# Optimization experiments

Measured on AMD Instinct MI355X. Metric: run time of the kernel, lower is better.

Reference implementation:

```python
import jax, jax.numpy as jnp
import numpy as np

DIM = 64

def conv2d_g2(x, w, b):
    # 3x3 conv, padding=1, groups=2, NCHW
    y = jax.lax.conv_general_dilated(x, w, (1, 1), [(1, 1), (1, 1)],
                                     dimension_numbers=('NCHW', 'OIHW', 'NCHW'),
                                     feature_group_count=2)
    return y + b[None, :, None, None]

def bilinear_gather(x, py, px):
    # x: [B,C,H,W]; py,px: [B,K,H,W] float sample coords -> [B,K,H,W,C]
    B, C, H, W = x.shape
    y0 = jnp.floor(py); x0 = jnp.floor(px)
    ly = py - y0; lx = px - x0
    hy = 1.0 - ly; hx = 1.0 - lx
    b_idx = jnp.arange(B)[:, None, None, None]
    def gather(yi, xi):
        valid = (yi >= 0) & (yi < H) & (xi >= 0) & (xi < W)
        yc = jnp.clip(yi, 0, H - 1).astype(jnp.int32)
        xc = jnp.clip(xi, 0, W - 1).astype(jnp.int32)
        v = x[b_idx, :, yc, xc]  # [B,K,H,W,C]
        return v * valid[..., None].astype(x.dtype)
    return (gather(y0, x0) * (hy * hx)[..., None]
            + gather(y0, x0 + 1) * (hy * lx)[..., None]
            + gather(y0 + 1, x0) * (ly * hx)[..., None]
            + gather(y0 + 1, x0 + 1) * (ly * lx)[..., None])

def deform_dw(x, offset, w, b, k, pad, dil):
    # depthwise (groups=C, offset_groups=1) deformable conv, stride 1
    B, C, H, W = x.shape
    K = k * k
    off = offset.reshape(B, K, 2, H, W)  # torchvision layout: (dy,dx) per kernel tap
    ky = jnp.repeat(jnp.arange(k), k).astype(x.dtype)   # [K]
    kx = jnp.tile(jnp.arange(k), k).astype(x.dtype)     # [K]
    base_y = jnp.arange(H, dtype=x.dtype)[None, None, :, None] - pad + dil * ky[None, :, None, None]
    base_x = jnp.arange(W, dtype=x.dtype)[None, None, None, :] - pad + dil * kx[None, :, None, None]
    py = base_y + off[:, :, 0]  # [B,K,H,W]
    px = base_x + off[:, :, 1]
    val = bilinear_gather(x, py, px)  # [B,K,H,W,C]
    return jnp.einsum('bkhwc,ck->bchw', val, w.reshape(C, K)) + b[None, :, None, None]

def lsk_forward(x, w_off3, b_off3, w_off2, b_off2, w7, b7, w5, b5):
    B, C, H, W = x.shape
    offset3 = conv2d_g2(x, w_off3, b_off3)            # [B,98,H,W]
    out1 = deform_dw(x, offset3, w7, b7, 7, 9, 3)     # [B,C,H,W]
    offset2 = conv2d_g2(x, w_off2, b_off2)            # [B,50,H,W]
    out2 = deform_dw(out1, offset2, w5, b5, 5, 6, 3)  # [B,C,H,W]
    feats = jnp.stack([out1, out2], axis=1)           # [B,2,C,H,W]
    gap = feats.mean(axis=(3, 4), keepdims=True)      # [B,2,C,1,1]
    attn = jax.nn.softmax(gap, axis=1)
    return jnp.sum(feats * attn, axis=1)              # [B,C,H,W]

def setup_inputs() -> dict:
    key = jax.random.key(0)
    ks = jax.random.split(key, 9)
    B, C, H, W = 4, DIM, 56, 56
    return {
        'x':      jax.random.normal(ks[0], (B, C, H, W), jnp.float32),
        'w_off3': jax.random.normal(ks[1], (98, C // 2, 3, 3), jnp.float32) * 0.05,
        'b_off3': jax.random.normal(ks[2], (98,), jnp.float32) * 0.05,
        'w_off2': jax.random.normal(ks[3], (50, C // 2, 3, 3), jnp.float32) * 0.05,
        'b_off2': jax.random.normal(ks[4], (50,), jnp.float32) * 0.05,
        'w7':     jax.random.normal(ks[5], (C, 1, 7, 7), jnp.float32) * 0.1,
        'b7':     jax.random.normal(ks[6], (C,), jnp.float32) * 0.05,
        'w5':     jax.random.normal(ks[7], (C, 1, 5, 5), jnp.float32) * 0.1,
        'b5':     jax.random.normal(ks[8], (C,), jnp.float32) * 0.05,
    }

def reference(x, w_off3, b_off3, w_off2, b_off2, w7, b7, w5, b5):
    return lsk_forward(x, w_off3, b_off3, w_off2, b_off2, w7, b7, w5, b5)
```

## Files before the change

### kernel.cpp

```cpp
#include <hip/hip_runtime.h>
#include <hip/hip_fp16.h>
#include <math.h>

#define HH 56
#define WW 56
#define CC 64
#define BB 4
#define HWA (HH*WW)

typedef _Float16 half8_t __attribute__((ext_vector_type(8)));
typedef _Float16 h2_t   __attribute__((ext_vector_type(2)));
typedef float f32x4_t __attribute__((ext_vector_type(4)));

#define PROWS 57
#define PSTRB (PROWS*57*64*4)
#define ROWSTRB (57*64*4)

__global__ __launch_bounds__(256)
void k_prep(const float* __restrict__ x,
            const float* __restrict__ w3, const float* __restrict__ w2,
            const float* __restrict__ b3, const float* __restrict__ b2,
            __half2* __restrict__ xp, _Float16* __restrict__ xh,
            _Float16* __restrict__ Wp, float* __restrict__ bbp) {
    int blk = blockIdx.x;
    int tid = threadIdx.x;
    if (blk < BB*56) {
        __shared__ float ld[64*57];
        int b = blk / 56, y = blk % 56;
        for (int i = tid; i < 64*56; i += 256) {
            int c = i / 56, col = i % 56;
            ld[c*57 + col] = x[((size_t)b*CC + c)*HWA + y*WW + col];
        }
        __syncthreads();
        for (int i = tid; i < 57*64; i += 256) {
            int j = i >> 6, c = i & 63;
            float lo = (j > 0)  ? ld[c*57 + j - 1] : 0.f;
            float hi = (j < 56) ? ld[c*57 + j]     : 0.f;
            xp[((size_t)(b*PROWS + y)*57 + j)*CC + c] = __floats2half2_rn(lo, hi);
        }
        _Float16* dst = xh + (((size_t)(b*2)*56 + y)*58)*32;
#pragma unroll
        for (int g = 0; g < 2; ++g) {
            for (int i = tid; i < 1856; i += 256) {
                int col = i >> 5, ic = i & 31;
                float v = (col >= 1 && col <= 56) ? ld[(g*32 + ic)*57 + col - 1] : 0.f;
                dst[(size_t)g*(56*58*32) + i] = (_Float16)v;
            }
        }
    } else {
        int i = (blk - BB*56)*256 + tid;
        if (i < 46080) {
            int j    = i & 7;
            int lane = (i >> 3) & 63;
            int mt   = (i >> 9) % 5;
            int kt   = (i / 2560) % 9;
            int g    = i / 23040;
            int m  = mt*16 + (lane & 15);
            int ic = (lane >> 4)*8 + j;
            int ky = kt/3, kx = kt%3;
            float v = 0.f;
            if (m < 49)      v = w3[((g*49 + m)*32 + ic)*9 + ky*3 + kx];
            else if (m < 74) v = w2[((g*25 + (m-49))*32 + ic)*9 + ky*3 + kx];
            Wp[i] = (_Float16)v;
        } else if (i < 46240) {
            int t = i - 46080; int g = t/80, m = t%80;
            float v = 0.f;
            if (m < 49)      v = b3[g*49 + m];
            else if (m < 74) v = b2[g*25 + (m-49)];
            bbp[t] = v;
        }
    }
}

__global__ __launch_bounds__(256)
void k_convmfma(const _Float16* __restrict__ xh, const _Float16* __restrict__ Wp,
                const float* __restrict__ bb,
                float* __restrict__ off3, float* __restrict__ off2) {
    __shared__ _Float16 tile[4][3*18*32];
    int blk = blockIdx.x;
    int iy = blk % 56;
    int g  = (blk / 56) & 1;
    int b  = blk / 112;
    int wv   = threadIdx.y;
    int lane = threadIdx.x;
    int n0 = wv * 16;

    const uint4* xs4 = (const uint4*)xh;
    uint4* tl4 = (uint4*)&tile[wv][0];
#pragma unroll
    for (int i = 0; i < 4; ++i) {
        int idx4 = i*64 + lane;
        if (idx4 < 216) {
            int ic4 = idx4 & 3;
            int seg = idx4 >> 2;
            int cl = seg % 18, r = seg / 18;
            int y = iy - 1 + r, col = n0 + cl;
            uint4 v = {0u, 0u, 0u, 0u};
            if (y >= 0 && y < 56 && col < 58)
                v = xs4[((((size_t)(b*2+g)*56 + y)*58 + col) << 2) + ic4];
            tl4[idx4] = v;
        }
    }
    __syncthreads();

    int nlo = lane & 15, khi = lane >> 4;
    f32x4_t acc[5];
#pragma unroll
    for (int mt = 0; mt < 5; ++mt) acc[mt] = (f32x4_t){0.f,0.f,0.f,0.f};

    const half8_t* wp8 = (const half8_t*)Wp;
#pragma unroll
    for (int kt = 0; kt < 9; ++kt) {
        int ky = kt/3, kx = kt%3;
        half8_t bfrag = *(const half8_t*)&tile[wv][((ky*18) + nlo + kx)*32 + khi*8];
#pragma unroll
        for (int mt = 0; mt < 5; ++mt) {
            half8_t afrag = wp8[(((size_t)g*9 + kt)*5 + mt)*64 + lane];
            acc[mt] = __builtin_amdgcn_mfma_f32_16x16x32_f16(afrag, bfrag, acc[mt], 0, 0, 0);
        }
    }

    int pixcol = n0 + nlo;
    if (pixcol < 56) {
        int pix = iy*WW + pixcol;
#pragma unroll
        for (int mt = 0; mt < 5; ++mt) {
#pragma unroll
            for (int r = 0; r < 4; ++r) {
                int m = mt*16 + khi*4 + r;
                if (m < 74) {
                    float val = acc[mt][r] + bb[g*80 + m];
                    if (m < 49)
                        off3[((size_t)b*98 + g*49 + m)*HWA + pix] = val;
                    else
                        off2[((size_t)b*50 + g*25 + (m-49))*HWA + pix] = val;
                }
            }
        }
    }
}

template<int K, int KS, int PAD, bool WP>
__global__ __launch_bounds__(256)
void k_deform(const _Float16* __restrict__ xp, const float* __restrict__ off,
              const float* __restrict__ wg, const float* __restrict__ bias,
              float* __restrict__ out, float* __restrict__ partial,
              _Float16* __restrict__ xpo) {
    __shared__ float lw[K*65];
    __shared__ float loffs[2*K][9];
    __shared__ float red[8][64];
    int tid = threadIdx.x + threadIdx.y*64;
    int blk = blockIdx.x;
    int xcd = blk & 7;
    int idx = blk >> 3;
    int b   = xcd >> 1;
    int hw0 = (xcd & 1)*(HWA/2) + idx*8;

    for (int i = tid; i < K*64; i += 256) {
        int c = i / K, t = i % K;
        lw[t*65 + c] = wg[i];
    }
    for (int i = tid; i < 4*K; i += 256) {
        int row = i >> 1, half = i & 1;
        float4 v = *(const float4*)&off[((size_t)b*2*K + row)*HWA + hw0 + half*4];
        loffs[row][half*4 + 0] = v.x; loffs[row][half*4 + 1] = v.y;
        loffs[row][half*4 + 2] = v.z; loffs[row][half*4 + 3] = v.w;
    }
    __syncthreads();

    int yp = threadIdx.y;
    int c  = threadIdx.x;

    int mx0 = 0, wz0 = 0, ww0 = 0;
    int mx1 = 0, wz1 = 0, ww1 = 0;
    if (c < K) {
        int t = c;
        int ky = t / KS, kx = t % KS;
#pragma unroll
        for (int s = 0; s < 2; ++s) {
            int p = yp + 4*s;
            int hw = hw0 + p;
            int h = hw / WW, w = hw % WW;
            float py = (float)(h - PAD + 3*ky) + loffs[2*t][p];
            float px = (float)(w - PAD + 3*kx) + loffs[2*t+1][p];
            float y0f = floorf(py), x0f = floorf(px);
            float ly = py - y0f, lx = px - x0f;
            float hy = 1.f - ly, hx = 1.f - lx;
            int y0 = (int)y0f, x0 = (int)x0f;
            int j = x0 + 1;
            bool jv = (j >= 0) && (j <= 56);
            int jc = jv ? j : 0;
            float s0 = ((y0   >= 0) && (y0   < HH) && jv) ? hy : 0.f;
            float s1 = ((y0+1 >= 0) && (y0+1 < HH) && jv) ? ly : 0.f;
            bool use1 = (s0 == 0.f);
            int rbase = use1 ? min(max(y0 + 1, 0), 55) : y0;
            float aw = use1 ? s1 : s0;
            float bw = use1 ? 0.f : s1;
            int mxv = (rbase*57 + jc)*(64*4);
            __half2 wah = __floats2half2_rn(aw*hx, aw*lx);
            __half2 wbh = __floats2half2_rn(bw*hx, bw*lx);
            if (s == 0) { mx0 = mxv; wz0 = *(int*)&wah; ww0 = *(int*)&wbh; }
            else        { mx1 = mxv; wz1 = *(int*)&wah; ww1 = *(int*)&wbh; }
        }
    }

    const char* xb = (const char*)xp + (size_t)b*PSTRB;
    float acc0 = 0.f, acc1 = 0.f;
#pragma unroll 8
    for (int t = 0; t < K; ++t) {
        int m0 = (int)__builtin_amdgcn_readlane(mx0, t);
        int z0 = (int)__builtin_amdgcn_readlane(wz0, t);
        int w0 = (int)__builtin_amdgcn_readlane(ww0, t);
        int m1 = (int)__builtin_amdgcn_readlane(mx1, t);
        int z1 = (int)__builtin_amdgcn_readlane(wz1, t);
        int w1 = (int)__builtin_amdgcn_readlane(ww1, t);
        const h2_t* r0p = (const h2_t*)(xb + m0);
        const h2_t* r1p = (const h2_t*)(xb + m0 + ROWSTRB);
        const h2_t* r2p = (const h2_t*)(xb + m1);
        const h2_t* r3p = (const h2_t*)(xb + m1 + ROWSTRB);
        h2_t r0a = r0p[c];
        h2_t r1a = r1p[c];
        h2_t r0b = r2p[c];
        h2_t r1b = r3p[c];
        float lwv = lw[t*65 + c];
        float v0 = __builtin_amdgcn_fdot2(r0a, *(h2_t*)&z0, 0.f, false);
        v0 = __builtin_amdgcn_fdot2(r1a, *(h2_t*)&w0, v0, false);
        float v1 = __builtin_amdgcn_fdot2(r0b, *(h2_t*)&z1, 0.f, false);
        v1 = __builtin_amdgcn_fdot2(r1b, *(h2_t*)&w1, v1, false);
        acc0 = fmaf(v0, lwv, acc0);
        acc1 = fmaf(v1, lwv, acc1);
    }
    float bs = bias[c];
    float val0 = acc0 + bs;
    float val1 = acc1 + bs;
    int hwA = hw0 + yp, hwB = hw0 + yp + 4;
    out[((size_t)b*HWA + hwA)*CC + c] = val0;
    out[((size_t)b*HWA + hwB)*CC + c] = val1;

    if (WP) {
#pragma unroll
        for (int s = 0; s < 2; ++s) {
            int hw = s ? hwB : hwA;
            float val = s ? val1 : val0;
            int y = hw / WW, w = hw % WW;
            _Float16* base = xpo + ((size_t)(b*PROWS + y)*57)*CC*2;
            _Float16 hv = (_Float16)val;
            base[((w    )*64 + c)*2 + 1] = hv;
            base[((w + 1)*64 + c)*2 + 0] = hv;
            if (w == 0)  base[(c)*2 + 0] = (_Float16)0.f;
            if (w == 55) base[((56)*64 + c)*2 + 1] = (_Float16)0.f;
        }
    }

    red[yp][c] = val0;
    red[yp + 4][c] = val1;
    __syncthreads();
    if (yp == 0) {
        float s = red[0][c] + red[1][c] + red[2][c] + red[3][c]
                + red[4][c] + red[5][c] + red[6][c] + red[7][c];
        partial[((size_t)b*(HWA/8) + (hw0 >> 3))*64 + c] = s;
    }
}

__global__ void k_gapA(const float* __restrict__ p1, const float* __restrict__ p2,
                       float* __restrict__ g2) {
    __shared__ float red[4][64];
    int blk = blockIdx.x;
    int chunk = blk % 14;
    int bf    = blk / 14;
    int b     = bf >> 1;
    const float* p = (bf & 1) ? p2 : p1;
    int tid = threadIdx.x;
    int c = tid & 63, s = tid >> 6;
    float sum = 0.f;
#pragma unroll
    for (int i = 0; i < 7; ++i) {
        int j = chunk*28 + s + 4*i;
        sum += p[((size_t)b*(HWA/8) + j)*64 + c];
    }
    red[s][c] = sum;
    __syncthreads();
    if (s == 0)
        g2[((size_t)bf*14 + chunk)*64 + c]
            = red[0][c] + red[1][c] + red[2][c] + red[3][c];
}

__global__ void k_combine(const float* __restrict__ o1, const float* __restrict__ o2,
                          const float* __restrict__ g2, float* __restrict__ out) {
    __shared__ float tile[64][65];
    __shared__ float ash[2][64];
    int blk = blockIdx.x;
    int b   = blk / (HWA/64);
    int t0  = (blk % (HWA/64)) * 64;
    int tid = threadIdx.x;

    if (tid < 64) {
        int cc = tid;
        float s1 = 0.f, s2 = 0.f;
#pragma unroll
        for (int k = 0; k < 14; ++k) {
            s1 += g2[((size_t)(b*2+0)*14 + k)*64 + cc];
            s2 += g2[((size_t)(b*2+1)*14 + k)*64 + cc];
        }
        s1 *= (1.f/HWA); s2 *= (1.f/HWA);
        float m  = fmaxf(s1, s2);
        float e1 = expf(s1 - m), e2 = expf(s2 - m);
        float a1 = e1 / (e1 + e2);
        ash[0][cc] = a1;
        ash[1][cc] = 1.f - a1;
    }
    __syncthreads();

    const float4* o14 = (const float4*)o1;
    const float4* o24 = (const float4*)o2;
#pragma unroll
    for (int i = 0; i < 4; ++i) {
        int f = i*256 + tid;
        int p = f >> 4, c4 = f & 15;
        size_t idx4 = (((size_t)b*HWA + t0 + p)*CC >> 2) + c4;
        float4 v1 = o14[idx4];
        float4 v2 = o24[idx4];
        float4 a1 = *(const float4*)&ash[0][c4*4];
        float4 a2 = *(const float4*)&ash[1][c4*4];
        tile[p][c4*4 + 0] = v1.x*a1.x + v2.x*a2.x;
        tile[p][c4*4 + 1] = v1.y*a1.y + v2.y*a2.y;
        tile[p][c4*4 + 2] = v1.z*a1.z + v2.z*a2.z;
        tile[p][c4*4 + 3] = v1.w*a1.w + v2.w*a2.w;
    }
    __syncthreads();
    int q = tid >> 6, p2 = tid & 63;
#pragma unroll
    for (int i = 0; i < 16; ++i) {
        int c2 = q + 4*i;
        out[((size_t)b*CC + c2)*HWA + t0 + p2] = tile[p2][c2];
    }
}

extern "C" void kernel_launch(void* const* d_in, const int* in_sizes, int n_in,
                              void* d_out, int out_size, void* d_ws, size_t ws_size,
                              hipStream_t stream) {
    const float* x      = (const float*)d_in[0];
    const float* w_off3 = (const float*)d_in[1];
    const float* b_off3 = (const float*)d_in[2];
    const float* w_off2 = (const float*)d_in[3];
    const float* b_off2 = (const float*)d_in[4];
    const float* w7     = (const float*)d_in[5];
    const float* b7     = (const float*)d_in[6];
    const float* w5     = (const float*)d_in[7];
    const float* b5     = (const float*)d_in[8];
    float* out = (float*)d_out;

    const size_t PAIRF = (size_t)BB*PROWS*57*64;
    float* ws    = (float*)d_ws;
    float* off3r = ws;
    float* off2r = off3r + 1229312;
    float* out1  = off2r + 627200;
    float* out2  = out1  + 802816;
    float* xp1f  = out2  + 802816;
    float* xp2f  = xp1f  + PAIRF;
    float* xhf   = xp2f  + PAIRF;
    float* part1 = xhf   + 415744;
    float* part2 = part1 + 100352;
    float* gpA   = part2 + 100352;
    float* wpf   = gpA   + 7168;
    float* bbp   = wpf   + 23040;
    __half2*  xp1 = (__half2*)xp1f;
    _Float16* xp2h = (_Float16*)xp2f;
    _Float16* xh  = (_Float16*)xhf;
    _Float16* Wp  = (_Float16*)wpf;
    size_t need = (size_t)(1229312 + 627200 + 802816*2 + 831744*2 + 415744
                           + 100352*2 + 7168 + 23040 + 160) * 4;
    if (ws_size < need) return;

    k_prep<<<BB*56 + 181, 256, 0, stream>>>(x, w_off3, w_off2, b_off3, b_off2,
                                            xp1, xh, Wp, bbp);
    k_convmfma<<<BB*2*56, dim3(64,4), 0, stream>>>(xh, Wp, bbp, off3r, off2r);
    k_deform<49,7,9,true><<<BB*(HWA/8), dim3(64,4), 0, stream>>>(
        (const _Float16*)xp1, off3r, w7, b7, out1, part1, xp2h);
    k_deform<25,5,6,false><<<BB*(HWA/8), dim3(64,4), 0, stream>>>(
        xp2h, off2r, w5, b5, out2, part2, nullptr);
    k_gapA<<<8*14, 256, 0, stream>>>(part1, part2, gpA);
    k_combine<<<BB*(HWA/64), 256, 0, stream>>>(out1, out2, gpA, out);
}
```

Before: 135.2 us.

## Fuse all stages into one persistent kernel with global atomic barriers

Merges the six separate launches (prep, offset conv, two deformable convs, GAP reduction, combine) into a single persistent kernel of 784 blocks. Stages are separated by a software grid barrier built on an atomic counter. The goal is to remove per-launch overhead and inter-kernel gaps. In exchange it adds barrier spin costs, requires every block to be co-resident (checked through an occupancy query, with the old multi-kernel path kept as a fallback), reduces the deform unroll, and retiles combine to 16 pixels per block.

```diff
diff --git a/kernel.cpp b/kernel.cpp
--- a/kernel.cpp
+++ b/kernel.cpp
@@ -16,68 +16,82 @@
 #define PSTRB (PROWS*57*64*4)
 #define ROWSTRB (57*64*4)
 
-__global__ __launch_bounds__(256)
-void k_prep(const float* __restrict__ x,
-            const float* __restrict__ w3, const float* __restrict__ w2,
-            const float* __restrict__ b3, const float* __restrict__ b2,
-            __half2* __restrict__ xp, _Float16* __restrict__ xh,
-            _Float16* __restrict__ Wp, float* __restrict__ bbp) {
-    int blk = blockIdx.x;
-    int tid = threadIdx.x;
-    if (blk < BB*56) {
-        __shared__ float ld[64*57];
-        int b = blk / 56, y = blk % 56;
-        for (int i = tid; i < 64*56; i += 256) {
-            int c = i / 56, col = i % 56;
-            ld[c*57 + col] = x[((size_t)b*CC + c)*HWA + y*WW + col];
-        }
-        __syncthreads();
-        for (int i = tid; i < 57*64; i += 256) {
-            int j = i >> 6, c = i & 63;
-            float lo = (j > 0)  ? ld[c*57 + j - 1] : 0.f;
-            float hi = (j < 56) ? ld[c*57 + j]     : 0.f;
-            xp[((size_t)(b*PROWS + y)*57 + j)*CC + c] = __floats2half2_rn(lo, hi);
-        }
-        _Float16* dst = xh + (((size_t)(b*2)*56 + y)*58)*32;
-#pragma unroll
-        for (int g = 0; g < 2; ++g) {
-            for (int i = tid; i < 1856; i += 256) {
-                int col = i >> 5, ic = i & 31;
-                float v = (col >= 1 && col <= 56) ? ld[(g*32 + ic)*57 + col - 1] : 0.f;
-                dst[(size_t)g*(56*58*32) + i] = (_Float16)v;
-            }
-        }
-    } else {
-        int i = (blk - BB*56)*256 + tid;
-        if (i < 46080) {
-            int j    = i & 7;
-            int lane = (i >> 3) & 63;
-            int mt   = (i >> 9) % 5;
-            int kt   = (i / 2560) % 9;
-            int g    = i / 23040;
-            int m  = mt*16 + (lane & 15);
-            int ic = (lane >> 4)*8 + j;
-            int ky = kt/3, kx = kt%3;
-            float v = 0.f;
-            if (m < 49)      v = w3[((g*49 + m)*32 + ic)*9 + ky*3 + kx];
-            else if (m < 74) v = w2[((g*25 + (m-49))*32 + ic)*9 + ky*3 + kx];
-            Wp[i] = (_Float16)v;
-        } else if (i < 46240) {
-            int t = i - 46080; int g = t/80, m = t%80;
-            float v = 0.f;
-            if (m < 49)      v = b3[g*49 + m];
-            else if (m < 74) v = b2[g*25 + (m-49)];
-            bbp[t] = v;
-        }
-    }
-}
-
-__global__ __launch_bounds__(256)
-void k_convmfma(const _Float16* __restrict__ xh, const _Float16* __restrict__ Wp,
-                const float* __restrict__ bb,
-                float* __restrict__ off3, float* __restrict__ off2) {
-    __shared__ _Float16 tile[4][3*18*32];
-    int blk = blockIdx.x;
+#define NB 784
+
+__device__ __forceinline__ void gbar(int* cnt, int target) {
+    __syncthreads();
+    if (threadIdx.x == 0 && threadIdx.y == 0) {
+        __threadfence();
+        __hip_atomic_fetch_add(cnt, 1, __ATOMIC_ACQ_REL, __HIP_MEMORY_SCOPE_AGENT);
+        int spins = 0;
+        while (__hip_atomic_load(cnt, __ATOMIC_ACQUIRE, __HIP_MEMORY_SCOPE_AGENT) < target) {
+            __builtin_amdgcn_s_sleep(1);
+            if (++spins > (1 << 24)) break;
+        }
+        __threadfence();
+    }
+    __syncthreads();
+}
+
+
+__device__ void prep_row(int u, int tid, float* ld,
+                         const float* __restrict__ x,
+                         __half2* __restrict__ xp, _Float16* __restrict__ xh) {
+    int b = u / 56, y = u % 56;
+    for (int i = tid; i < 64*56; i += 256) {
+        int c = i / 56, col = i % 56;
+        ld[c*57 + col] = x[((size_t)b*CC + c)*HWA + y*WW + col];
+    }
+    __syncthreads();
+    for (int i = tid; i < 57*64; i += 256) {
+        int j = i >> 6, c = i & 63;
+        float lo = (j > 0)  ? ld[c*57 + j - 1] : 0.f;
+        float hi = (j < 56) ? ld[c*57 + j]     : 0.f;
+        xp[((size_t)(b*PROWS + y)*57 + j)*CC + c] = __floats2half2_rn(lo, hi);
+    }
+    _Float16* dst = xh + (((size_t)(b*2)*56 + y)*58)*32;
+#pragma unroll
+    for (int g = 0; g < 2; ++g) {
+        for (int i = tid; i < 1856; i += 256) {
+            int col = i >> 5, ic = i & 31;
+            float v = (col >= 1 && col <= 56) ? ld[(g*32 + ic)*57 + col - 1] : 0.f;
+            dst[(size_t)g*(56*58*32) + i] = (_Float16)v;
+        }
+    }
+}
+
+__device__ void pack_unit(int u, int tid,
+                          const float* __restrict__ w3, const float* __restrict__ w2,
+                          const float* __restrict__ b3, const float* __restrict__ b2,
+                          _Float16* __restrict__ Wp, float* __restrict__ bbp) {
+    int i = u*256 + tid;
+    if (i < 46080) {
+        int j    = i & 7;
+        int lane = (i >> 3) & 63;
+        int mt   = (i >> 9) % 5;
+        int kt   = (i / 2560) % 9;
+        int g    = i / 23040;
+        int m  = mt*16 + (lane & 15);
+        int ic = (lane >> 4)*8 + j;
+        int ky = kt/3, kx = kt%3;
+        float v = 0.f;
+        if (m < 49)      v = w3[((g*49 + m)*32 + ic)*9 + ky*3 + kx];
+        else if (m < 74) v = w2[((g*25 + (m-49))*32 + ic)*9 + ky*3 + kx];
+        Wp[i] = (_Float16)v;
+    } else if (i < 46240) {
+        int t = i - 46080; int g = t/80, m = t%80;
+        float v = 0.f;
+        if (m < 49)      v = b3[g*49 + m];
+        else if (m < 74) v = b2[g*25 + (m-49)];
+        bbp[t] = v;
+    }
+}
+
+__device__ void conv_unit(int blk, char* smemraw,
+                          const _Float16* __restrict__ xh, const _Float16* __restrict__ Wp,
+                          const float* __restrict__ bb,
+                          float* __restrict__ off3, float* __restrict__ off2) {
+    _Float16 (*tile)[3*18*32] = (_Float16(*)[3*18*32])smemraw;
     int iy = blk % 56;
     int g  = (blk / 56) & 1;
     int b  = blk / 112;
@@ -119,6 +133,7 @@
             acc[mt] = __builtin_amdgcn_mfma_f32_16x16x32_f16(afrag, bfrag, acc[mt], 0, 0, 0);
         }
     }
+    __syncthreads();
 
     int pixcol = n0 + nlo;
     if (pixcol < 56) {
@@ -141,16 +156,15 @@
 }
 
 template<int K, int KS, int PAD, bool WP>
-__global__ __launch_bounds__(256)
-void k_deform(const _Float16* __restrict__ xp, const float* __restrict__ off,
-              const float* __restrict__ wg, const float* __restrict__ bias,
-              float* __restrict__ out, float* __restrict__ partial,
-              _Float16* __restrict__ xpo) {
-    __shared__ float lw[K*65];
-    __shared__ float loffs[2*K][9];
-    __shared__ float red[8][64];
+__device__ void deform_unit(int blk, char* smemraw,
+                            const _Float16* __restrict__ xp, const float* __restrict__ off,
+                            const float* __restrict__ wg, const float* __restrict__ bias,
+                            float* __restrict__ out, float* __restrict__ partial,
+                            _Float16* __restrict__ xpo) {
+    float* lw = (float*)smemraw;
+    float (*loffs)[9] = (float(*)[9])(lw + K*65);
+    float (*red)[64]  = (float(*)[64])(lw + K*65 + 2*K*9);
     int tid = threadIdx.x + threadIdx.y*64;
-    int blk = blockIdx.x;
     int xcd = blk & 7;
     int idx = blk >> 3;
     int b   = xcd >> 1;
@@ -206,7 +220,7 @@
 
     const char* xb = (const char*)xp + (size_t)b*PSTRB;
     float acc0 = 0.f, acc1 = 0.f;
-#pragma unroll 8
+#pragma unroll 4
     for (int t = 0; t < K; ++t) {
         int m0 = (int)__builtin_amdgcn_readlane(mx0, t);
         int z0 = (int)__builtin_amdgcn_readlane(wz0, t);
@@ -262,15 +276,14 @@
     }
 }
 
-__global__ void k_gapA(const float* __restrict__ p1, const float* __restrict__ p2,
-                       float* __restrict__ g2) {
-    __shared__ float red[4][64];
-    int blk = blockIdx.x;
+__device__ void gap_unit(int blk, int tid, float* redraw,
+                         const float* __restrict__ p1, const float* __restrict__ p2,
+                         float* __restrict__ g2) {
+    float (*red)[64] = (float(*)[64])redraw;
     int chunk = blk % 14;
     int bf    = blk / 14;
     int b     = bf >> 1;
     const float* p = (bf & 1) ? p2 : p1;
-    int tid = threadIdx.x;
     int c = tid & 63, s = tid >> 6;
     float sum = 0.f;
 #pragma unroll
@@ -285,56 +298,138 @@
             = red[0][c] + red[1][c] + red[2][c] + red[3][c];
 }
 
-__global__ void k_combine(const float* __restrict__ o1, const float* __restrict__ o2,
+__device__ void combine16(int blk, int tid, float* smemf,
+                          const float* __restrict__ o1, const float* __restrict__ o2,
                           const float* __restrict__ g2, float* __restrict__ out) {
-    __shared__ float tile[64][65];
-    __shared__ float ash[2][64];
-    int blk = blockIdx.x;
-    int b   = blk / (HWA/64);
-    int t0  = (blk % (HWA/64)) * 64;
-    int tid = threadIdx.x;
+    float* ash = smemf;
+    float (*tile)[65] = (float(*)[65])(smemf + 128);
+    int b  = blk / 196;
+    int t0 = (blk % 196) * 16;
 
     if (tid < 64) {
-        int cc = tid;
         float s1 = 0.f, s2 = 0.f;
 #pragma unroll
         for (int k = 0; k < 14; ++k) {
-            s1 += g2[((size_t)(b*2+0)*14 + k)*64 + cc];
-            s2 += g2[((size_t)(b*2+1)*14 + k)*64 + cc];
+            s1 += g2[((size_t)(b*2+0)*14 + k)*64 + tid];
+            s2 += g2[((size_t)(b*2+1)*14 + k)*64 + tid];
         }
         s1 *= (1.f/HWA); s2 *= (1.f/HWA);
         float m  = fmaxf(s1, s2);
         float e1 = expf(s1 - m), e2 = expf(s2 - m);
         float a1 = e1 / (e1 + e2);
-        ash[0][cc] = a1;
-        ash[1][cc] = 1.f - a1;
-    }
-    __syncthreads();
-
-    const float4* o14 = (const float4*)o1;
-    const float4* o24 = (const float4*)o2;
+        ash[tid]      = a1;
+        ash[64 + tid] = 1.f - a1;
+    }
+    __syncthreads();
+
+    int p  = tid >> 4, c4 = tid & 15;
+    size_t idx4 = ((size_t)b*HWA + t0 + p)*16 + c4;
+    float4 v1 = ((const float4*)o1)[idx4];
+    float4 v2 = ((const float4*)o2)[idx4];
+    tile[p][c4*4 + 0] = v1.x*ash[c4*4+0] + v2.x*ash[64+c4*4+0];
+    tile[p][c4*4 + 1] = v1.y*ash[c4*4+1] + v2.y*ash[64+c4*4+1];
+    tile[p][c4*4 + 2] = v1.z*ash[c4*4+2] + v2.z*ash[64+c4*4+2];
+    tile[p][c4*4 + 3] = v1.w*ash[c4*4+3] + v2.w*ash[64+c4*4+3];
+    __syncthreads();
+
+    int px = tid & 15, c0 = tid >> 4;
 #pragma unroll
     for (int i = 0; i < 4; ++i) {
-        int f = i*256 + tid;
-        int p = f >> 4, c4 = f & 15;
-        size_t idx4 = (((size_t)b*HWA + t0 + p)*CC >> 2) + c4;
-        float4 v1 = o14[idx4];
-        float4 v2 = o24[idx4];
-        float4 a1 = *(const float4*)&ash[0][c4*4];
-        float4 a2 = *(const float4*)&ash[1][c4*4];
-        tile[p][c4*4 + 0] = v1.x*a1.x + v2.x*a2.x;
-        tile[p][c4*4 + 1] = v1.y*a1.y + v2.y*a2.y;
-        tile[p][c4*4 + 2] = v1.z*a1.z + v2.z*a2.z;
-        tile[p][c4*4 + 3] = v1.w*a1.w + v2.w*a2.w;
-    }
-    __syncthreads();
-    int q = tid >> 6, p2 = tid & 63;
-#pragma unroll
-    for (int i = 0; i < 16; ++i) {
-        int c2 = q + 4*i;
-        out[((size_t)b*CC + c2)*HWA + t0 + p2] = tile[p2][c2];
-    }
-}
+        int c = c0 + 16*i;
+        out[((size_t)b*CC + c)*HWA + t0 + px] = tile[px][c];
+    }
+}
+
+
+struct KP {
+    const float *x, *w3, *b3, *w2, *b2, *w7, *b7, *w5, *b5;
+    float *out;
+    float *off3, *off2, *out1, *out2;
+    __half2 *xp1; _Float16 *xp2, *xh, *Wp;
+    float *part1, *part2, *gpA, *bbp;
+    int *cnt;
+};
+
+__global__ __launch_bounds__(256, 4)
+void k_fused(KP p) {
+    __shared__ __align__(16) char smem[18432];
+    int blk = blockIdx.x;
+    int tid = threadIdx.x + threadIdx.y*64;
+
+    if (blk < BB*56)
+        prep_row(blk, tid, (float*)smem, p.x, p.xp1, p.xh);
+    else if (blk < BB*56 + 181)
+        pack_unit(blk - BB*56, tid, p.w3, p.w2, p.b3, p.b2, p.Wp, p.bbp);
+    gbar(p.cnt, 1*NB);
+
+    if (blk < BB*2*56)
+        conv_unit(blk, smem, p.xh, p.Wp, p.bbp, p.off3, p.off2);
+    gbar(p.cnt, 2*NB);
+
+    deform_unit<49,7,9,true>(blk, smem, (const _Float16*)p.xp1, p.off3, p.w7, p.b7,
+                             p.out1, p.part1, p.xp2);
+    __syncthreads();
+    deform_unit<49,7,9,true>(blk + NB, smem, (const _Float16*)p.xp1, p.off3, p.w7, p.b7,
+                             p.out1, p.part1, p.xp2);
+    gbar(p.cnt, 3*NB);
+
+    deform_unit<25,5,6,false>(blk, smem, p.xp2, p.off2, p.w5, p.b5,
+                              p.out2, p.part2, nullptr);
+    __syncthreads();
+    deform_unit<25,5,6,false>(blk + NB, smem, p.xp2, p.off2, p.w5, p.b5,
+                              p.out2, p.part2, nullptr);
+    gbar(p.cnt, 4*NB);
+
+    if (blk < 112)
+        gap_unit(blk, tid, (float*)smem, p.part1, p.part2, p.gpA);
+    gbar(p.cnt, 5*NB);
+
+    combine16(blk, tid, (float*)smem, p.out1, p.out2, p.gpA, p.out);
+}
+
+
+__global__ __launch_bounds__(256)
+void k_prep(const float* __restrict__ x,
+            const float* __restrict__ w3, const float* __restrict__ w2,
+            const float* __restrict__ b3, const float* __restrict__ b2,
+            __half2* __restrict__ xp, _Float16* __restrict__ xh,
+            _Float16* __restrict__ Wp, float* __restrict__ bbp) {
+    __shared__ __align__(16) char smem[14592];
+    int blk = blockIdx.x, tid = threadIdx.x;
+    if (blk < BB*56) prep_row(blk, tid, (float*)smem, x, xp, xh);
+    else             pack_unit(blk - BB*56, tid, w3, w2, b3, b2, Wp, bbp);
+}
+
+__global__ __launch_bounds__(256)
+void k_convmfma(const _Float16* __restrict__ xh, const _Float16* __restrict__ Wp,
+                const float* __restrict__ bb,
+                float* __restrict__ off3, float* __restrict__ off2) {
+    __shared__ __align__(16) char smem[13824];
+    conv_unit(blockIdx.x, smem, xh, Wp, bb, off3, off2);
+}
+
+template<int K, int KS, int PAD, bool WP>
+__global__ __launch_bounds__(256)
+void k_deform(const _Float16* __restrict__ xp, const float* __restrict__ off,
+              const float* __restrict__ wg, const float* __restrict__ bias,
+              float* __restrict__ out, float* __restrict__ partial,
+              _Float16* __restrict__ xpo) {
+    __shared__ __align__(16) char smem[18432];
+    deform_unit<K,KS,PAD,WP>(blockIdx.x, smem, xp, off, wg, bias, out, partial, xpo);
+}
+
+__global__ void k_gapA(const float* __restrict__ p1, const float* __restrict__ p2,
+                       float* __restrict__ g2) {
+    __shared__ float red[4][64];
+    gap_unit(blockIdx.x, threadIdx.x, &red[0][0], p1, p2, g2);
+}
+
+__global__ void k_combine16(const float* __restrict__ o1, const float* __restrict__ o2,
+                            const float* __restrict__ g2, float* __restrict__ out) {
+    __shared__ float smemf[128 + 16*65];
+    combine16(blockIdx.x, threadIdx.x, smemf, o1, o2, g2, out);
+}
+
 
 extern "C" void kernel_launch(void* const* d_in, const int* in_sizes, int n_in,
                               void* d_out, int out_size, void* d_ws, size_t ws_size,
@@ -364,21 +459,40 @@
     float* gpA   = part2 + 100352;
     float* wpf   = gpA   + 7168;
     float* bbp   = wpf   + 23040;
-    __half2*  xp1 = (__half2*)xp1f;
+    float* cntf  = bbp   + 160;
+    __half2*  xp1  = (__half2*)xp1f;
     _Float16* xp2h = (_Float16*)xp2f;
-    _Float16* xh  = (_Float16*)xhf;
-    _Float16* Wp  = (_Float16*)wpf;
+    _Float16* xh   = (_Float16*)xhf;
+    _Float16* Wp   = (_Float16*)wpf;
+    int* cnt = (int*)cntf;
     size_t need = (size_t)(1229312 + 627200 + 802816*2 + 831744*2 + 415744
-                           + 100352*2 + 7168 + 23040 + 160) * 4;
+                           + 100352*2 + 7168 + 23040 + 160 + 16) * 4;
     if (ws_size < need) return;
 
-    k_prep<<<BB*56 + 181, 256, 0, stream>>>(x, w_off3, w_off2, b_off3, b_off2,
-                                            xp1, xh, Wp, bbp);
-    k_convmfma<<<BB*2*56, dim3(64,4), 0, stream>>>(xh, Wp, bbp, off3r, off2r);
-    k_deform<49,7,9,true><<<BB*(HWA/8), dim3(64,4), 0, stream>>>(
-        (const _Float16*)xp1, off3r, w7, b7, out1, part1, xp2h);
-    k_deform<25,5,6,false><<<BB*(HWA/8), dim3(64,4), 0, stream>>>(
-        xp2h, off2r, w5, b5, out2, part2, nullptr);
-    k_gapA<<<8*14, 256, 0, stream>>>(part1, part2, gpA);
-    k_combine<<<BB*(HWA/64), 256, 0, stream>>>(out1, out2, gpA, out);
-}
+    int occ = 0;
+    hipError_t qe = hipOccupancyMaxActiveBlocksPerMultiprocessor(&occ, k_fused, 256, 0);
+    bool fused_ok = (qe == hipSuccess) && (occ * 256 >= NB);
+
+    if (fused_ok) {
+        KP kp;
+        kp.x = x; kp.w3 = w_off3; kp.b3 = b_off3; kp.w2 = w_off2; kp.b2 = b_off2;
+        kp.w7 = w7; kp.b7 = b7; kp.w5 = w5; kp.b5 = b5;
+        kp.out = out;
+        kp.off3 = off3r; kp.off2 = off2r; kp.out1 = out1; kp.out2 = out2;
+        kp.xp1 = xp1; kp.xp2 = xp2h; kp.xh = xh; kp.Wp = Wp;
+        kp.part1 = part1; kp.part2 = part2; kp.gpA = gpA; kp.bbp = bbp;
+        kp.cnt = cnt;
+        hipMemsetAsync(cnt, 0, 64, stream);
+        k_fused<<<NB, dim3(64,4), 0, stream>>>(kp);
+    } else {
+        k_prep<<<BB*56 + 181, 256, 0, stream>>>(x, w_off3, w_off2, b_off3, b_off2,
+                                                xp1, xh, Wp, bbp);
+        k_convmfma<<<BB*2*56, dim3(64,4), 0, stream>>>(xh, Wp, bbp, off3r, off2r);
+        k_deform<49,7,9,true><<<BB*(HWA/8), dim3(64,4), 0, stream>>>(
+            (const _Float16*)xp1, off3r, w7, b7, out1, part1, xp2h);
+        k_deform<25,5,6,false><<<BB*(HWA/8), dim3(64,4), 0, stream>>>(
+            xp2h, off2r, w5, b5, out2, part2, nullptr);
+        k_gapA<<<8*14, 256, 0, stream>>>(part1, part2, gpA);
+        k_combine16<<<BB*196, 256, 0, stream>>>(out1, out2, gpA, out);
+    }
+}
```

Result: slower. 144.0 us (+6.5%).

## Vectorize deform gathers to 16-byte loads per lane and shrink combine tiles

Applied to the files above, without the earlier changes.

The deformable conv inner loop now has each lane issue one 16-byte load covering 4 channels of one row for one pixel, with 16-lane groups split across pixel and row. The two row contributions are merged with a cross-lane shuffle, and results are written as float4 through shared memory. This replaces four 4-byte gathers per lane per tap and cuts memory instructions, at the cost of a shuffle and an extra barrier. The combine kernel uses 16-pixel tiles, giving four times as many blocks for more parallelism but shorter coalesced NCHW store runs.

```diff
diff --git a/kernel.cpp b/kernel.cpp
--- a/kernel.cpp
+++ b/kernel.cpp
@@ -146,7 +146,7 @@
               const float* __restrict__ wg, const float* __restrict__ bias,
               float* __restrict__ out, float* __restrict__ partial,
               _Float16* __restrict__ xpo) {
-    __shared__ float lw[K*65];
+    __shared__ float lwf[K*64];
     __shared__ float loffs[2*K][9];
     __shared__ float red[8][64];
     int tid = threadIdx.x + threadIdx.y*64;
@@ -157,8 +157,8 @@
     int hw0 = (xcd & 1)*(HWA/2) + idx*8;
 
     for (int i = tid; i < K*64; i += 256) {
-        int c = i / K, t = i % K;
-        lw[t*65 + c] = wg[i];
+        int cch = i / K, t = i % K;
+        lwf[t*64 + cch] = wg[i];
     }
     for (int i = tid; i < 4*K; i += 256) {
         int row = i >> 1, half = i & 1;
@@ -204,40 +204,53 @@
         }
     }
 
+    int grp = c >> 4, li = c & 15;
+    int voffb = (grp & 1) * ROWSTRB + li * 16;
+    bool pix1 = (grp & 2) != 0;
+    bool rowB = (grp & 1) != 0;
     const char* xb = (const char*)xp + (size_t)b*PSTRB;
-    float acc0 = 0.f, acc1 = 0.f;
+
+    f32x4_t acc = (f32x4_t){0.f, 0.f, 0.f, 0.f};
 #pragma unroll 8
     for (int t = 0; t < K; ++t) {
         int m0 = (int)__builtin_amdgcn_readlane(mx0, t);
+        int m1 = (int)__builtin_amdgcn_readlane(mx1, t);
         int z0 = (int)__builtin_amdgcn_readlane(wz0, t);
         int w0 = (int)__builtin_amdgcn_readlane(ww0, t);
-        int m1 = (int)__builtin_amdgcn_readlane(mx1, t);
         int z1 = (int)__builtin_amdgcn_readlane(wz1, t);
         int w1 = (int)__builtin_amdgcn_readlane(ww1, t);
-        const h2_t* r0p = (const h2_t*)(xb + m0);
-        const h2_t* r1p = (const h2_t*)(xb + m0 + ROWSTRB);
-        const h2_t* r2p = (const h2_t*)(xb + m1);
-        const h2_t* r3p = (const h2_t*)(xb + m1 + ROWSTRB);
-        h2_t r0a = r0p[c];
-        h2_t r1a = r1p[c];
-        h2_t r0b = r2p[c];
-        h2_t r1b = r3p[c];
-        float lwv = lw[t*65 + c];
-        float v0 = __builtin_amdgcn_fdot2(r0a, *(h2_t*)&z0, 0.f, false);
-        v0 = __builtin_amdgcn_fdot2(r1a, *(h2_t*)&w0, v0, false);
-        float v1 = __builtin_amdgcn_fdot2(r0b, *(h2_t*)&z1, 0.f, false);
-        v1 = __builtin_amdgcn_fdot2(r1b, *(h2_t*)&w1, v1, false);
-        acc0 = fmaf(v0, lwv, acc0);
-        acc1 = fmaf(v1, lwv, acc1);
-    }
-    float bs = bias[c];
-    float val0 = acc0 + bs;
-    float val1 = acc1 + bs;
+        int msel = pix1 ? m1 : m0;
+        int wsel = pix1 ? (rowB ? w1 : z1) : (rowB ? w0 : z0);
+        uint4 d = *(const uint4*)(xb + msel + voffb);
+        float4 lv = *(const float4*)&lwf[t*64 + 4*li];
+        h2_t wh = *(h2_t*)&wsel;
+        acc[0] = fmaf(__builtin_amdgcn_fdot2(*(h2_t*)&d.x, wh, 0.f, false), lv.x, acc[0]);
+        acc[1] = fmaf(__builtin_amdgcn_fdot2(*(h2_t*)&d.y, wh, 0.f, false), lv.y, acc[1]);
+        acc[2] = fmaf(__builtin_amdgcn_fdot2(*(h2_t*)&d.z, wh, 0.f, false), lv.z, acc[2]);
+        acc[3] = fmaf(__builtin_amdgcn_fdot2(*(h2_t*)&d.w, wh, 0.f, false), lv.w, acc[3]);
+    }
+
+    float4 bs4 = *(const float4*)&bias[4*li];
+    float o0 = acc[0] + __shfl_xor(acc[0], 16) + bs4.x;
+    float o1 = acc[1] + __shfl_xor(acc[1], 16) + bs4.y;
+    float o2 = acc[2] + __shfl_xor(acc[2], 16) + bs4.z;
+    float o3 = acc[3] + __shfl_xor(acc[3], 16) + bs4.w;
+
     int hwA = hw0 + yp, hwB = hw0 + yp + 4;
-    out[((size_t)b*HWA + hwA)*CC + c] = val0;
-    out[((size_t)b*HWA + hwB)*CC + c] = val1;
+    if (grp == 0) {
+        float4 o = {o0, o1, o2, o3};
+        *(float4*)&red[yp][4*li] = o;
+        *(float4*)&out[((size_t)b*HWA + hwA)*CC + 4*li] = o;
+    } else if (grp == 2) {
+        float4 o = {o0, o1, o2, o3};
+        *(float4*)&red[yp + 4][4*li] = o;
+        *(float4*)&out[((size_t)b*HWA + hwB)*CC + 4*li] = o;
+    }
+    __syncthreads();
 
     if (WP) {
+        float val0 = red[yp][c];
+        float val1 = red[yp + 4][c];
 #pragma unroll
         for (int s = 0; s < 2; ++s) {
             int hw = s ? hwB : hwA;
@@ -252,9 +265,6 @@
         }
     }
 
-    red[yp][c] = val0;
-    red[yp + 4][c] = val1;
-    __syncthreads();
     if (yp == 0) {
         float s = red[0][c] + red[1][c] + red[2][c] + red[3][c]
                 + red[4][c] + red[5][c] + red[6][c] + red[7][c];
@@ -285,54 +295,46 @@
             = red[0][c] + red[1][c] + red[2][c] + red[3][c];
 }
 
-__global__ void k_combine(const float* __restrict__ o1, const float* __restrict__ o2,
-                          const float* __restrict__ g2, float* __restrict__ out) {
-    __shared__ float tile[64][65];
-    __shared__ float ash[2][64];
-    int blk = blockIdx.x;
-    int b   = blk / (HWA/64);
-    int t0  = (blk % (HWA/64)) * 64;
+__global__ void k_combine16(const float* __restrict__ o1, const float* __restrict__ o2,
+                            const float* __restrict__ g2, float* __restrict__ out) {
+    __shared__ float ash[128];
+    __shared__ float tile[16][65];
+    int blk = blockIdx.x;
     int tid = threadIdx.x;
+    int b  = blk / 196;
+    int t0 = (blk % 196) * 16;
 
     if (tid < 64) {
-        int cc = tid;
         float s1 = 0.f, s2 = 0.f;
 #pragma unroll
         for (int k = 0; k < 14; ++k) {
-            s1 += g2[((size_t)(b*2+0)*14 + k)*64 + cc];
-            s2 += g2[((size_t)(b*2+1)*14 + k)*64 + cc];
+            s1 += g2[((size_t)(b*2+0)*14 + k)*64 + tid];
+            s2 += g2[((size_t)(b*2+1)*14 + k)*64 + tid];
         }
         s1 *= (1.f/HWA); s2 *= (1.f/HWA);
         float m  = fmaxf(s1, s2);
         float e1 = expf(s1 - m), e2 = expf(s2 - m);
         float a1 = e1 / (e1 + e2);
-        ash[0][cc] = a1;
-        ash[1][cc] = 1.f - a1;
-    }
-    __syncthreads();
-
-    const float4* o14 = (const float4*)o1;
-    const float4* o24 = (const float4*)o2;
+        ash[tid]      = a1;
+        ash[64 + tid] = 1.f - a1;
+    }
+    __syncthreads();
+
+    int p  = tid >> 4, c4 = tid & 15;
+    size_t idx4 = ((size_t)b*HWA + t0 + p)*16 + c4;
+    float4 v1 = ((const float4*)o1)[idx4];
+    float4 v2 = ((const float4*)o2)[idx4];
+    tile[p][c4*4 + 0] = v1.x*ash[c4*4+0] + v2.x*ash[64+c4*4+0];
+    tile[p][c4*4 + 1] = v1.y*ash[c4*4+1] + v2.y*ash[64+c4*4+1];
+    tile[p][c4*4 + 2] = v1.z*ash[c4*4+2] + v2.z*ash[64+c4*4+2];
+    tile[p][c4*4 + 3] = v1.w*ash[c4*4+3] + v2.w*ash[64+c4*4+3];
+    __syncthreads();
+
+    int px = tid & 15, c0 = tid >> 4;
 #pragma unroll
     for (int i = 0; i < 4; ++i) {
-        int f = i*256 + tid;
-        int p = f >> 4, c4 = f & 15;
-        size_t idx4 = (((size_t)b*HWA + t0 + p)*CC >> 2) + c4;
-        float4 v1 = o14[idx4];
-        float4 v2 = o24[idx4];
-        float4 a1 = *(const float4*)&ash[0][c4*4];
-        float4 a2 = *(const float4*)&ash[1][c4*4];
-        tile[p][c4*4 + 0] = v1.x*a1.x + v2.x*a2.x;
-        tile[p][c4*4 + 1] = v1.y*a1.y + v2.y*a2.y;
-        tile[p][c4*4 + 2] = v1.z*a1.z + v2.z*a2.z;
-        tile[p][c4*4 + 3] = v1.w*a1.w + v2.w*a2.w;
-    }
-    __syncthreads();
-    int q = tid >> 6, p2 = tid & 63;
-#pragma unroll
-    for (int i = 0; i < 16; ++i) {
-        int c2 = q + 4*i;
-        out[((size_t)b*CC + c2)*HWA + t0 + p2] = tile[p2][c2];
+        int c = c0 + 16*i;
+        out[((size_t)b*CC + c)*HWA + t0 + px] = tile[px][c];
     }
 }
 
@@ -364,10 +366,10 @@
     float* gpA   = part2 + 100352;
     float* wpf   = gpA   + 7168;
     float* bbp   = wpf   + 23040;
-    __half2*  xp1 = (__half2*)xp1f;
+    __half2*  xp1  = (__half2*)xp1f;
     _Float16* xp2h = (_Float16*)xp2f;
-    _Float16* xh  = (_Float16*)xhf;
-    _Float16* Wp  = (_Float16*)wpf;
+    _Float16* xh   = (_Float16*)xhf;
+    _Float16* Wp   = (_Float16*)wpf;
     size_t need = (size_t)(1229312 + 627200 + 802816*2 + 831744*2 + 415744
                            + 100352*2 + 7168 + 23040 + 160) * 4;
     if (ws_size < need) return;
@@ -380,5 +382,5 @@
     k_deform<25,5,6,false><<<BB*(HWA/8), dim3(64,4), 0, stream>>>(
         xp2h, off2r, w5, b5, out2, part2, nullptr);
     k_gapA<<<8*14, 256, 0, stream>>>(part1, part2, gpA);
-    k_combine<<<BB*(HWA/64), 256, 0, stream>>>(out1, out2, gpA, out);
-}
+    k_combine16<<<BB*196, 256, 0, stream>>>(out1, out2, gpA, out);
+}
```

New measurement: 143.1 us. 1.06x slower.
